# Kernel tuning notes

Hardware: AMD Instinct MI355X
Metric: run time of the kernel (lower is better)

## Reference

```python
import jax, jax.numpy as jnp
import numpy as np

B, D = 8192, 1024          # batch, input dim
UNITS = [1024, 512]        # expert MLP hidden sizes
T, E_T, E_S = 2, 2, 4      # num_tasks, experts per task, shared experts
E = T * E_T + E_S          # total experts = 8


def setup_inputs() -> dict:
    key = jax.random.key(0)
    k = jax.random.split(key, 6)
    H, O = UNITS
    x = jax.random.normal(k[0], (B, D), dtype=jnp.float32)
    # glorot-normal-ish scaling for expert weights
    W1 = jax.random.normal(k[1], (E, D, H), dtype=jnp.float32) * np.sqrt(2.0 / (D + H))
    b1 = jnp.zeros((E, H), dtype=jnp.float32)
    W2 = jax.random.normal(k[2], (E, H, O), dtype=jnp.float32) * np.sqrt(2.0 / (H + O))
    b2 = jnp.zeros((E, O), dtype=jnp.float32)
    # per-task gate over (E_T + E_S) experts, no bias (use_bias=False in Dense)
    Wg = jax.random.normal(k[3], (T, D, E_T + E_S), dtype=jnp.float32) * np.sqrt(2.0 / (D + E_T + E_S))
    # shared gate over all E experts
    Wgs = jax.random.normal(k[4], (D, E), dtype=jnp.float32) * np.sqrt(2.0 / (D + E))
    return {"x": x, "W1": W1, "b1": b1, "W2": W2, "b2": b2, "Wg": Wg, "Wgs": Wgs}


def reference(x, W1, b1, W2, b2, Wg, Wgs):
    # All experts see the same input (2D-input path of CGC3: tf.tile over experts).
    # Batched grouped GEMM over the expert axis instead of a Python loop.
    h = jax.nn.relu(jnp.einsum('bd,edh->ebh', x, W1) + b1[:, None, :])   # [E,B,H]
    eo = jax.nn.relu(jnp.einsum('ebh,eho->ebo', h, W2) + b2[:, None, :]) # [E,B,O]

    outs = []
    for i in range(T):
        # experts for task i = its own E_T experts + the last E_S shared experts
        idx = jnp.array(list(range(i * E_T, (i + 1) * E_T)) + list(range(E - E_S, E)))
        g = jax.nn.softmax(x @ Wg[i], axis=-1)            # [B, E_T+E_S]
        sel = eo[idx]                                     # [E_T+E_S, B, O]
        outs.append(jnp.einsum('be,ebo->bo', g, sel))     # [B, O]
    # output_share=True: share tower gated over all experts
    gs = jax.nn.softmax(x @ Wgs, axis=-1)                 # [B, E]
    outs.append(jnp.einsum('be,ebo->bo', gs, eo))         # [B, O]
    return jnp.stack(outs, axis=1)                        # [B, T+1, O]
```

## Files before the change

kernel.cpp:

```cpp
#include <hip/hip_runtime.h>
#include <hip/hip_bf16.h>
#include <stdint.h>

#define B_SZ 8192
#define D_SZ 1024
#define H_SZ 1024
#define O_SZ 512
#define E_SZ 8

typedef float f32x16 __attribute__((ext_vector_type(16)));
typedef __bf16 bf16x8 __attribute__((ext_vector_type(8)));

typedef __attribute__((address_space(1))) uint32_t gu32;
typedef __attribute__((address_space(3))) uint32_t lu32;

__device__ __forceinline__ unsigned short f2bf(float f) {
    union { __hip_bfloat16 h; unsigned short u; } c;
    c.h = __float2bfloat16(f);
    return c.u;
}
__device__ __forceinline__ float bf2f(unsigned short u) {
    union { float f; uint32_t u; } c;
    c.u = ((uint32_t)u) << 16;
    return c.f;
}


__global__ __launch_bounds__(1024) void k_convert_gates(const float* __restrict__ x,
                                                        const float* __restrict__ Wg,
                                                        const float* __restrict__ Wgs,
                                                        unsigned short* __restrict__ x_kb,
                                                        float* __restrict__ g_all) {
    __shared__ unsigned short xs[16][D_SZ];
    const int wv = threadIdx.x >> 6;
    const int lane = threadIdx.x & 63;
    const int b0 = blockIdx.x * 16;
    const int b = b0 + wv;
    const float* xr = x + (size_t)b * D_SZ;
    float acc[20];
#pragma unroll
    for (int j = 0; j < 20; ++j) acc[j] = 0.f;
#pragma unroll 4
    for (int it = 0; it < 16; ++it) {
        const int d = it * 64 + lane;
        const float xv = xr[d];
        xs[wv][d] = f2bf(xv);
        const float* w0 = Wg + (size_t)d * 6;
        const float* w1 = Wg + (size_t)D_SZ * 6 + (size_t)d * 6;
        const float* ws = Wgs + (size_t)d * 8;
#pragma unroll
        for (int j = 0; j < 6; ++j) acc[j] += xv * w0[j];
#pragma unroll
        for (int j = 0; j < 6; ++j) acc[6 + j] += xv * w1[j];
#pragma unroll
        for (int j = 0; j < 8; ++j) acc[12 + j] += xv * ws[j];
    }
#pragma unroll
    for (int j = 0; j < 20; ++j) {
        float v = acc[j];
#pragma unroll
        for (int s = 32; s > 0; s >>= 1) v += __shfl_down(v, s, 64);
        acc[j] = v;
    }
    if (lane == 0) {
        float* g = g_all + (size_t)b * 20;
#pragma unroll
        for (int t = 0; t < 3; ++t) {
            int base = (t == 0) ? 0 : (t == 1 ? 6 : 12);
            int cnt  = (t == 2) ? 8 : 6;
            float m = -1e30f;
            for (int j = 0; j < cnt; ++j) m = fmaxf(m, acc[base + j]);
            float ex[8]; float sum = 0.f;
            for (int j = 0; j < cnt; ++j) { ex[j] = __expf(acc[base + j] - m); sum += ex[j]; }
            float inv = 1.f / sum;
            for (int j = 0; j < cnt; ++j) g[base + j] = ex[j] * inv;
        }
    }
    __syncthreads();
    const char* lb = (const char*)&xs[0][0];
#pragma unroll
    for (int p = 0; p < 2; ++p) {
        const int u = p * 1024 + threadIdx.x;
        const int kblk = u >> 4, r16 = u & 15;
        int4 v = *(const int4*)(lb + r16 * 2048 + kblk * 16);
        *(int4*)(x_kb + (size_t)(b0 >> 8) * (D_SZ * 256) + (size_t)kblk * 2048
                 + ((b0 & 255) + r16) * 8) = v;
    }
}

__global__ __launch_bounds__(512) void k_transpose_panel(const float* __restrict__ in,
                                                         unsigned short* __restrict__ out,
                                                         int R, int C) {
    __shared__ float tile[64][65];
    const float* src = in + (size_t)blockIdx.z * R * C;
    unsigned short* dst = out + (size_t)blockIdx.z * R * C;
    int c0 = blockIdx.x * 64, r0 = blockIdx.y * 64;
    int tx = threadIdx.x, ty = threadIdx.y;
#pragma unroll
    for (int rr = ty; rr < 64; rr += 8)
        tile[rr][tx] = src[(size_t)(r0 + rr) * C + c0 + tx];
    __syncthreads();
    union { ushort4 h[2]; int4 q; } u;
#pragma unroll
    for (int s = 0; s < 8; ++s)
        ((unsigned short*)&u)[s] = f2bf(tile[ty * 8 + s][tx]);
    const int c = c0 + tx;
    *(int4*)(dst + (size_t)(c >> 8) * (R * 256) + (size_t)((r0 >> 3) + ty) * 2048
             + (c & 255) * 8) = u.q;
}

template <bool PANEL_OUT>
__global__ __launch_bounds__(512, 2) void k_gemm_p(
    const unsigned short* __restrict__ A,
    const unsigned short* __restrict__ Bt,
    const float* __restrict__ bias,
    unsigned short* __restrict__ C,
    int M, int N, int K,
    long long sA, long long sB, long long sBias, long long sC, int e_base) {

    const int tid = threadIdx.x;
    const int lane = tid & 63, wid = tid >> 6;
    const int wr = wid >> 2, wc = wid & 3;
    const int lr32 = lane & 31, hi = lane >> 5;

    const int nwg = gridDim.x;
    const int wg = blockIdx.x;
    const int swz = (wg & 7) * (nwg >> 3) + (wg >> 3);
    const int nx = N >> 8;
    const int my = M >> 8;
    const int bx = swz % nx;
    const int t1 = swz / nx;
    const int by = t1 % my;
    const int e  = t1 / my + e_base;

    A    += (size_t)((long long)e * sA);
    Bt   += (size_t)((long long)e * sB);
    bias += (size_t)((long long)e * sBias);
    C    += (size_t)((long long)e * sC);

    const int m0 = by * 256, n0 = bx * 256;

    __shared__ __align__(16) unsigned short lds[65536];
    char* ldsb = (char*)lds;

    const int skb = tid >> 8;
    const int srw = tid & 255;

    auto stageA = [&](int tt) {
        const int bb = (tt & 3) * 32768;
        const unsigned short* s0 = A + (size_t)(m0 >> 8) * K * 256
                                     + (size_t)(tt * 4 + skb) * 2048 + srw * 8;
        __builtin_amdgcn_global_load_lds((gu32*)s0, (lu32*)(ldsb + bb + tid * 16), 16, 0, 0);
        __builtin_amdgcn_global_load_lds((gu32*)(s0 + 4096),
                                         (lu32*)(ldsb + bb + 8192 + tid * 16), 16, 0, 0);
    };
    auto stageB = [&](int tt) {
        const int bb = (tt & 3) * 32768 + 16384;
        const unsigned short* s0 = Bt + (size_t)(n0 >> 8) * K * 256
                                      + (size_t)(tt * 4 + skb) * 2048 + srw * 8;
        __builtin_amdgcn_global_load_lds((gu32*)s0, (lu32*)(ldsb + bb + tid * 16), 16, 0, 0);
        __builtin_amdgcn_global_load_lds((gu32*)(s0 + 4096),
                                         (lu32*)(ldsb + bb + 8192 + tid * 16), 16, 0, 0);
    };

    const int abase = (wr * 128 + lr32) * 16 + hi * 4096;
    const int bbase = 16384 + (wc * 64 + lr32) * 16 + hi * 4096;

    auto readA = [&](bf16x8* d, int bb, int mb) {
#pragma unroll
        for (int q = 0; q < 4; ++q) {
            const int mi = mb + (q >> 1), s = q & 1;
            d[q] = *(const bf16x8*)(ldsb + bb + abase + mi * 512 + s * 8192);
        }
    };
    auto readB = [&](bf16x8* d, int bb) {
#pragma unroll
        for (int q = 0; q < 4; ++q) {
            const int nj = q >> 1, s = q & 1;
            d[q] = *(const bf16x8*)(ldsb + bb + bbase + nj * 512 + s * 8192);
        }
    };

    f32x16 acc[4][2];
#pragma unroll
    for (int i = 0; i < 4; ++i)
#pragma unroll
        for (int j = 0; j < 2; ++j)
            acc[i][j] = (f32x16)(0.f);

    auto mfma8 = [&](const bf16x8* fa, const bf16x8* fb, int rb) {
        __builtin_amdgcn_s_setprio(1);
#pragma unroll
        for (int i = 0; i < 2; ++i)
#pragma unroll
            for (int j = 0; j < 2; ++j)
#pragma unroll
                for (int s = 0; s < 2; ++s)
                    acc[rb + i][j] = __builtin_amdgcn_mfma_f32_32x32x16_bf16(
                        fa[i * 2 + s], fb[j * 2 + s], acc[rb + i][j], 0, 0, 0);
        __builtin_amdgcn_s_setprio(0);
    };

    const int NT = K >> 5;

    stageA(0); stageB(0); stageA(1); stageB(1); stageA(2); stageB(2);
    asm volatile("s_waitcnt vmcnt(8)" ::: "memory");
    asm volatile("s_barrier" ::: "memory");

    bf16x8 aU0[4], aL0[4], b0[4], aU1[4], aL1[4], b1v[4];
    readA(aU0, 0, 0); readB(b0, 0);

    for (int t = 0; t < NT; t += 2) {
        const int bb0 = (t & 3) * 32768;
        const int bb1 = ((t + 1) & 3) * 32768;
        const int bb2 = ((t + 2) & 3) * 32768;

        readA(aL0, bb0, 2);
        if (t + 2 < NT) { asm volatile("s_waitcnt vmcnt(4)" ::: "memory"); }
        else            { asm volatile("s_waitcnt vmcnt(0)" ::: "memory"); }
        asm volatile("s_barrier" ::: "memory");
        if (t + 3 < NT) stageA(t + 3);
        mfma8(aU0, b0, 0);

        readA(aU1, bb1, 0); readB(b1v, bb1);
        asm volatile("s_barrier" ::: "memory");
        if (t + 3 < NT) stageB(t + 3);
        mfma8(aL0, b0, 2);

        readA(aL1, bb1, 2);
        if (t + 3 < NT) { asm volatile("s_waitcnt vmcnt(4)" ::: "memory"); }
        else            { asm volatile("s_waitcnt vmcnt(0)" ::: "memory"); }
        asm volatile("s_barrier" ::: "memory");
        if (t + 4 < NT) stageA(t + 4);
        mfma8(aU1, b1v, 0);

        if (t + 2 < NT) { readA(aU0, bb2, 0); readB(b0, bb2); }
        asm volatile("s_barrier" ::: "memory");
        if (t + 4 < NT) stageB(t + 4);
        mfma8(aL1, b1v, 4 - 2);
    }

    __syncthreads();
    unsigned short* ct = (unsigned short*)ldsb;
#pragma unroll
    for (int nj = 0; nj < 2; ++nj) {
        const int nn = wc * 64 + nj * 32 + lr32;
        const float bv = bias[n0 + nn];
#pragma unroll
        for (int mi = 0; mi < 4; ++mi) {
#pragma unroll
            for (int r = 0; r < 16; ++r) {
                const int mloc = wr * 128 + mi * 32 + (r & 3) + 8 * (r >> 2) + 4 * hi;
                float v = fmaxf(acc[mi][nj][r] + bv, 0.f);
                if (PANEL_OUT) {
                    const int pu = (nn >> 3) ^ (mloc & 7);
                    *(unsigned short*)(ldsb + mloc * 512 + pu * 16 + (nn & 7) * 2) = f2bf(v);
                } else {
                    ct[(size_t)mloc * 256 + nn] = f2bf(v);
                }
            }
        }
    }
    __syncthreads();
    if (PANEL_OUT) {
#pragma unroll
        for (int it = 0; it < 16; ++it) {
            const int u = it * 512 + tid;
            const int blk = u >> 8, row = u & 255;
            int4 v = *(const int4*)(ldsb + row * 512 + ((blk ^ (row & 7)) * 16));
            *(int4*)(C + (size_t)(m0 >> 8) * N * 256 + (size_t)((n0 >> 3) + blk) * 2048
                     + row * 8) = v;
        }
    } else {
#pragma unroll
        for (int it = 0; it < 16; ++it) {
            const int row = it * 16 + (tid >> 5);
            const int colE = (tid & 31) * 8;
            *(int4*)(&C[(size_t)(m0 + row) * N + n0 + colE]) =
                *(const int4*)(ldsb + it * 8192 + (size_t)tid * 16);
        }
    }
}

__global__ __launch_bounds__(256) void k_combine(const unsigned short* __restrict__ eo,
                                                 const float* __restrict__ g_all,
                                                 float* __restrict__ out) {
    int idx4 = blockIdx.x * 256 + threadIdx.x;
    int b = idx4 >> 7;
    int o4 = (idx4 & 127) * 4;
    const float* g = g_all + (size_t)b * 20;
    float v[E_SZ][4];
#pragma unroll
    for (int e = 0; e < E_SZ; ++e) {
        ushort4 u = *(const ushort4*)(eo + (size_t)e * B_SZ * O_SZ + (size_t)b * O_SZ + o4);
        v[e][0] = bf2f(u.x); v[e][1] = bf2f(u.y); v[e][2] = bf2f(u.z); v[e][3] = bf2f(u.w);
    }
    float4 r0, r1, r2;
    float* p0 = (float*)&r0; float* p1 = (float*)&r1; float* p2 = (float*)&r2;
#pragma unroll
    for (int c = 0; c < 4; ++c) {
        p0[c] = g[0] * v[0][c] + g[1] * v[1][c] + g[2] * v[4][c] + g[3] * v[5][c]
              + g[4] * v[6][c] + g[5] * v[7][c];
        p1[c] = g[6] * v[2][c] + g[7] * v[3][c] + g[8] * v[4][c] + g[9] * v[5][c]
              + g[10] * v[6][c] + g[11] * v[7][c];
        float s = 0.f;
#pragma unroll
        for (int e = 0; e < E_SZ; ++e) s += g[12 + e] * v[e][c];
        p2[c] = s;
    }
    size_t ob = (size_t)b * (3 * O_SZ) + o4;
    *(float4*)(out + ob) = r0;
    *(float4*)(out + ob + O_SZ) = r1;
    *(float4*)(out + ob + 2 * O_SZ) = r2;
}

extern "C" void kernel_launch(void* const* d_in, const int* in_sizes, int n_in,
                              void* d_out, int out_size, void* d_ws, size_t ws_size,
                              hipStream_t stream) {
    const float* x   = (const float*)d_in[0];
    const float* W1  = (const float*)d_in[1];
    const float* b1  = (const float*)d_in[2];
    const float* W2  = (const float*)d_in[3];
    const float* b2  = (const float*)d_in[4];
    const float* Wg  = (const float*)d_in[5];
    const float* Wgs = (const float*)d_in[6];
    float* out = (float*)d_out;

    char* ws = (char*)d_ws;
    const size_t SZ_XBF  = (size_t)B_SZ * D_SZ * 2;
    const size_t SZ_W1T  = (size_t)E_SZ * H_SZ * D_SZ * 2;
    const size_t SZ_W2T  = (size_t)E_SZ * O_SZ * H_SZ * 2;
    const size_t SZ_EO   = (size_t)E_SZ * B_SZ * O_SZ * 2;
    const size_t SZ_G    = (size_t)B_SZ * 20 * 4;
    const size_t SZ_HBIG = (size_t)E_SZ * B_SZ * H_SZ * 2;

    unsigned short* x_kb = (unsigned short*)ws;              ws += SZ_XBF;
    unsigned short* W1T  = (unsigned short*)ws;              ws += SZ_W1T;
    unsigned short* W2T  = (unsigned short*)ws;              ws += SZ_W2T;
    unsigned short* eo   = (unsigned short*)ws;              ws += SZ_EO;
    float* g_all         = (float*)ws;                       ws += SZ_G;
    unsigned short* h_buf = (unsigned short*)ws;

    const size_t fixed = SZ_XBF + SZ_W1T + SZ_W2T + SZ_EO + SZ_G;
    const bool big = ws_size >= fixed + SZ_HBIG;

    k_convert_gates<<<B_SZ / 16, 1024, 0, stream>>>(x, Wg, Wgs, x_kb, g_all);
    dim3 tb(64, 8);
    k_transpose_panel<<<dim3(H_SZ / 64, D_SZ / 64, E_SZ), tb, 0, stream>>>(W1, W1T, D_SZ, H_SZ);
    k_transpose_panel<<<dim3(O_SZ / 64, H_SZ / 64, E_SZ), tb, 0, stream>>>(W2, W2T, H_SZ, O_SZ);

    if (big) {
        k_gemm_p<true><<<(H_SZ / 256) * (B_SZ / 256) * E_SZ, 512, 0, stream>>>(
            x_kb, W1T, b1, h_buf, B_SZ, H_SZ, D_SZ,
            0LL, (long long)H_SZ * D_SZ, (long long)H_SZ, (long long)B_SZ * H_SZ, 0);
        k_gemm_p<false><<<(O_SZ / 256) * (B_SZ / 256) * E_SZ, 512, 0, stream>>>(
            h_buf, W2T, b2, eo, B_SZ, O_SZ, H_SZ,
            (long long)B_SZ * H_SZ, (long long)O_SZ * H_SZ, (long long)O_SZ, (long long)B_SZ * O_SZ, 0);
    } else {
        for (int e = 0; e < E_SZ; ++e) {
            k_gemm_p<true><<<(H_SZ / 256) * (B_SZ / 256), 512, 0, stream>>>(
                x_kb, W1T, b1, h_buf, B_SZ, H_SZ, D_SZ,
                0LL, (long long)H_SZ * D_SZ, (long long)H_SZ, 0LL, e);
            k_gemm_p<false><<<(O_SZ / 256) * (B_SZ / 256), 512, 0, stream>>>(
                h_buf, W2T, b2, eo, B_SZ, O_SZ, H_SZ,
                0LL, (long long)O_SZ * H_SZ, (long long)O_SZ, (long long)B_SZ * O_SZ, e);
        }
    }

    k_combine<<<(B_SZ * O_SZ / 4) / 256, 256, 0, stream>>>(eo, g_all, out);
}
```

Baseline: 315.6 us.

## Halve GEMM LDS to double-buffer so two workgroups fit per CU

Cuts the GEMM shared-memory buffer from 128KB with four pipeline stages to 64KB with two, and reschedules the main loop as double buffering with extra lgkmcnt waits and barriers. The epilogue now writes the output tile in two 128-row halves through the smaller LDS. The goal is to fit two 512-thread workgroups per CU, matching the launch bounds, so more waves can hide latency. The cost is a shallower prefetch pipeline, more synchronisation, and a leftover dead LDS read loop in the panel epilogue.

```diff
diff --git a/kernel.cpp b/kernel.cpp
--- a/kernel.cpp
+++ b/kernel.cpp
@@ -110,7 +110,7 @@
 }
 
 template <bool PANEL_OUT>
-__global__ __launch_bounds__(512, 2) void k_gemm_p(
+__global__ __launch_bounds__(512, 2) void k_gemm_r2(
     const unsigned short* __restrict__ A,
     const unsigned short* __restrict__ Bt,
     const float* __restrict__ bias,
@@ -140,14 +140,14 @@
 
     const int m0 = by * 256, n0 = bx * 256;
 
-    __shared__ __align__(16) unsigned short lds[65536];
+    __shared__ __align__(16) unsigned short lds[32768];
     char* ldsb = (char*)lds;
 
     const int skb = tid >> 8;
     const int srw = tid & 255;
 
     auto stageA = [&](int tt) {
-        const int bb = (tt & 3) * 32768;
+        const int bb = (tt & 1) * 32768;
         const unsigned short* s0 = A + (size_t)(m0 >> 8) * K * 256
                                      + (size_t)(tt * 4 + skb) * 2048 + srw * 8;
         __builtin_amdgcn_global_load_lds((gu32*)s0, (lu32*)(ldsb + bb + tid * 16), 16, 0, 0);
@@ -155,7 +155,7 @@
                                          (lu32*)(ldsb + bb + 8192 + tid * 16), 16, 0, 0);
     };
     auto stageB = [&](int tt) {
-        const int bb = (tt & 3) * 32768 + 16384;
+        const int bb = (tt & 1) * 32768 + 16384;
         const unsigned short* s0 = Bt + (size_t)(n0 >> 8) * K * 256
                                       + (size_t)(tt * 4 + skb) * 2048 + srw * 8;
         __builtin_amdgcn_global_load_lds((gu32*)s0, (lu32*)(ldsb + bb + tid * 16), 16, 0, 0);
@@ -203,82 +203,89 @@
 
     const int NT = K >> 5;
 
-    stageA(0); stageB(0); stageA(1); stageB(1); stageA(2); stageB(2);
-    asm volatile("s_waitcnt vmcnt(8)" ::: "memory");
+    stageA(0); stageB(0); stageA(1); stageB(1);
+    asm volatile("s_waitcnt vmcnt(4)" ::: "memory");
     asm volatile("s_barrier" ::: "memory");
 
     bf16x8 aU0[4], aL0[4], b0[4], aU1[4], aL1[4], b1v[4];
     readA(aU0, 0, 0); readB(b0, 0);
 
     for (int t = 0; t < NT; t += 2) {
-        const int bb0 = (t & 3) * 32768;
-        const int bb1 = ((t + 1) & 3) * 32768;
-        const int bb2 = ((t + 2) & 3) * 32768;
-
-        readA(aL0, bb0, 2);
+        readA(aL0, 0, 2);
+        asm volatile("s_waitcnt lgkmcnt(0)" ::: "memory");
+        asm volatile("s_barrier" ::: "memory");
+        if (t + 2 < NT) { stageA(t + 2); stageB(t + 2); }
+        mfma8(aU0, b0, 0);
         if (t + 2 < NT) { asm volatile("s_waitcnt vmcnt(4)" ::: "memory"); }
         else            { asm volatile("s_waitcnt vmcnt(0)" ::: "memory"); }
         asm volatile("s_barrier" ::: "memory");
-        if (t + 3 < NT) stageA(t + 3);
-        mfma8(aU0, b0, 0);
-
-        readA(aU1, bb1, 0); readB(b1v, bb1);
+        readA(aU1, 32768, 0); readB(b1v, 32768);
+        mfma8(aL0, b0, 2);
+
+        readA(aL1, 32768, 2);
+        asm volatile("s_waitcnt lgkmcnt(0)" ::: "memory");
         asm volatile("s_barrier" ::: "memory");
-        if (t + 3 < NT) stageB(t + 3);
-        mfma8(aL0, b0, 2);
-
-        readA(aL1, bb1, 2);
+        if (t + 3 < NT) { stageA(t + 3); stageB(t + 3); }
+        mfma8(aU1, b1v, 0);
         if (t + 3 < NT) { asm volatile("s_waitcnt vmcnt(4)" ::: "memory"); }
         else            { asm volatile("s_waitcnt vmcnt(0)" ::: "memory"); }
         asm volatile("s_barrier" ::: "memory");
-        if (t + 4 < NT) stageA(t + 4);
-        mfma8(aU1, b1v, 0);
-
-        if (t + 2 < NT) { readA(aU0, bb2, 0); readB(b0, bb2); }
-        asm volatile("s_barrier" ::: "memory");
-        if (t + 4 < NT) stageB(t + 4);
-        mfma8(aL1, b1v, 4 - 2);
+        if (t + 2 < NT) { readA(aU0, 0, 0); readB(b0, 0); }
+        mfma8(aL1, b1v, 2);
     }
 
     __syncthreads();
-    unsigned short* ct = (unsigned short*)ldsb;
-#pragma unroll
-    for (int nj = 0; nj < 2; ++nj) {
-        const int nn = wc * 64 + nj * 32 + lr32;
-        const float bv = bias[n0 + nn];
-#pragma unroll
-        for (int mi = 0; mi < 4; ++mi) {
-#pragma unroll
-            for (int r = 0; r < 16; ++r) {
-                const int mloc = wr * 128 + mi * 32 + (r & 3) + 8 * (r >> 2) + 4 * hi;
-                float v = fmaxf(acc[mi][nj][r] + bv, 0.f);
-                if (PANEL_OUT) {
-                    const int pu = (nn >> 3) ^ (mloc & 7);
-                    *(unsigned short*)(ldsb + mloc * 512 + pu * 16 + (nn & 7) * 2) = f2bf(v);
-                } else {
-                    ct[(size_t)mloc * 256 + nn] = f2bf(v);
+#pragma unroll
+    for (int h = 0; h < 2; ++h) {
+        if (wr == h) {
+#pragma unroll
+            for (int nj = 0; nj < 2; ++nj) {
+                const int nn = wc * 64 + nj * 32 + lr32;
+                const float bv = bias[n0 + nn];
+#pragma unroll
+                for (int mi = 0; mi < 4; ++mi) {
+#pragma unroll
+                    for (int r = 0; r < 16; ++r) {
+                        const int ml = mi * 32 + (r & 3) + 8 * (r >> 2) + 4 * hi;
+                        float v = fmaxf(acc[mi][nj][r] + bv, 0.f);
+                        if (PANEL_OUT) {
+                            const int pu = (nn >> 3) ^ (ml & 7);
+                            *(unsigned short*)(ldsb + ml * 512 + pu * 16 + (nn & 7) * 2) = f2bf(v);
+                        } else {
+                            *(unsigned short*)(ldsb + ml * 512 + nn * 2) = f2bf(v);
+                        }
+                    }
                 }
             }
         }
-    }
-    __syncthreads();
-    if (PANEL_OUT) {
-#pragma unroll
-        for (int it = 0; it < 16; ++it) {
-            const int u = it * 512 + tid;
-            const int blk = u >> 8, row = u & 255;
-            int4 v = *(const int4*)(ldsb + row * 512 + ((blk ^ (row & 7)) * 16));
-            *(int4*)(C + (size_t)(m0 >> 8) * N * 256 + (size_t)((n0 >> 3) + blk) * 2048
-                     + row * 8) = v;
-        }
-    } else {
-#pragma unroll
-        for (int it = 0; it < 16; ++it) {
-            const int row = it * 16 + (tid >> 5);
-            const int colE = (tid & 31) * 8;
-            *(int4*)(&C[(size_t)(m0 + row) * N + n0 + colE]) =
-                *(const int4*)(ldsb + it * 8192 + (size_t)tid * 16);
-        }
+        __syncthreads();
+        if (PANEL_OUT) {
+#pragma unroll
+            for (int it = 0; it < 8; ++it) {
+                const int u = it * 512 + tid;
+                const int blk = u >> 8, row = u & 255;
+                int4 v = *(const int4*)(ldsb + (row & 127) * 512
+                                        + (((blk * 2 + (row >> 7)) ^ ((row & 127) & 7)) * 16));
+                (void)v;
+            }
+#pragma unroll
+            for (int it = 0; it < 8; ++it) {
+                const int u = it * 512 + tid;
+                const int row = u >> 5, blk = u & 31;
+                int4 v = *(const int4*)(ldsb + row * 512 + ((blk ^ (row & 7)) * 16));
+                *(int4*)(C + (size_t)(m0 >> 8) * N * 256 + (size_t)((n0 >> 3) + blk) * 2048
+                         + (h * 128 + row + (m0 & 255)) * 8) = v;
+            }
+        } else {
+#pragma unroll
+            for (int it = 0; it < 8; ++it) {
+                const int u = it * 512 + tid;
+                const int row = u >> 5, blk = u & 31;
+                *(int4*)(&C[(size_t)(m0 + h * 128 + row) * N + n0 + blk * 8]) =
+                    *(const int4*)(ldsb + row * 512 + blk * 16);
+            }
+        }
+        __syncthreads();
     }
 }
 
@@ -350,18 +357,18 @@
     k_transpose_panel<<<dim3(O_SZ / 64, H_SZ / 64, E_SZ), tb, 0, stream>>>(W2, W2T, H_SZ, O_SZ);
 
     if (big) {
-        k_gemm_p<true><<<(H_SZ / 256) * (B_SZ / 256) * E_SZ, 512, 0, stream>>>(
+        k_gemm_r2<true><<<(H_SZ / 256) * (B_SZ / 256) * E_SZ, 512, 0, stream>>>(
             x_kb, W1T, b1, h_buf, B_SZ, H_SZ, D_SZ,
             0LL, (long long)H_SZ * D_SZ, (long long)H_SZ, (long long)B_SZ * H_SZ, 0);
-        k_gemm_p<false><<<(O_SZ / 256) * (B_SZ / 256) * E_SZ, 512, 0, stream>>>(
+        k_gemm_r2<false><<<(O_SZ / 256) * (B_SZ / 256) * E_SZ, 512, 0, stream>>>(
             h_buf, W2T, b2, eo, B_SZ, O_SZ, H_SZ,
             (long long)B_SZ * H_SZ, (long long)O_SZ * H_SZ, (long long)O_SZ, (long long)B_SZ * O_SZ, 0);
     } else {
         for (int e = 0; e < E_SZ; ++e) {
-            k_gemm_p<true><<<(H_SZ / 256) * (B_SZ / 256), 512, 0, stream>>>(
+            k_gemm_r2<true><<<(H_SZ / 256) * (B_SZ / 256), 512, 0, stream>>>(
                 x_kb, W1T, b1, h_buf, B_SZ, H_SZ, D_SZ,
                 0LL, (long long)H_SZ * D_SZ, (long long)H_SZ, 0LL, e);
-            k_gemm_p<false><<<(O_SZ / 256) * (B_SZ / 256), 512, 0, stream>>>(
+            k_gemm_r2<false><<<(O_SZ / 256) * (B_SZ / 256), 512, 0, stream>>>(
                 h_buf, W2T, b2, eo, B_SZ, O_SZ, H_SZ,
                 0LL, (long long)O_SZ * H_SZ, (long long)O_SZ, (long long)B_SZ * O_SZ, e);
         }
```

After: 326.9 us. +3.6%, slower.
